# Kernel tuning notes

Hardware: AMD Instinct MI355X
Metric: run time of the kernel (lower is better)

The kernel has to match this reference:

```python
import jax, jax.numpy as jnp
import numpy as np

DIM = 2048
N_HEADS = 16
HEAD_DIM = DIM // N_HEADS
EPS = 1e-6


def setup_inputs() -> dict:
    key = jax.random.key(0)
    k1, k2, k3, k4, k5 = jax.random.split(key, 5)
    B, S = 2, 2048
    x = jax.random.normal(k1, (B, S, DIM), dtype=jnp.float32)
    cos = jax.random.uniform(k2, (S, HEAD_DIM), dtype=jnp.float32)
    sin = jax.random.uniform(k3, (S, HEAD_DIM), dtype=jnp.float32)
    # torch nn.Linear convention: weight [out_features, in_features], y = x @ W.T
    W_qkv = jax.random.normal(k4, (3 * DIM, DIM), dtype=jnp.float32) * 0.02
    W_proj = jax.random.normal(k5, (DIM, DIM), dtype=jnp.float32) * 0.02
    return {"x": x, "cos": cos, "sin": sin, "W_qkv": W_qkv, "W_proj": W_proj}


def _apply_rope(x, cos, sin):
    # x: [B,H,S,D], cos/sin: [S,D]; rotate interleaved even/odd pairs
    x1, x2 = x[..., ::2], x[..., 1::2]
    c = cos[:, ::2][None, None]  # [1,1,S,D/2]
    s = sin[:, ::2][None, None]
    y1 = x1 * c - x2 * s
    y2 = x1 * s + x2 * c
    return jnp.stack([y1, y2], axis=-1).reshape(x.shape)


def _rms_norm(x):
    # per-head RMS normalization over last dim, no learned scale
    return x * jax.lax.rsqrt(jnp.mean(x * x, axis=-1, keepdims=True) + EPS)


def reference(x, cos, sin, W_qkv, W_proj):
    b, s, d = x.shape
    qkv = jnp.einsum('bsd,ed->bse', x, W_qkv)  # [B,S,3*dim]
    q, k, v = jnp.split(qkv, 3, axis=-1)
    # [B,S,dim] -> [B,H,S,Dh]
    def to_heads(t):
        return t.reshape(b, s, N_HEADS, HEAD_DIM).transpose(0, 2, 1, 3)
    q, k, v = to_heads(q), to_heads(k), to_heads(v)
    q = _apply_rope(_rms_norm(q), cos, sin)
    k = _apply_rope(_rms_norm(k), cos, sin)
    scale = 1.0 / jnp.sqrt(jnp.asarray(HEAD_DIM, dtype=x.dtype))
    scores = jnp.einsum('bhqd,bhkd->bhqk', q, k) * scale  # [B,H,S,S]
    attn = jax.nn.softmax(scores, axis=-1)
    out = jnp.einsum('bhqk,bhkd->bhqd', attn, v)  # [B,H,S,Dh]
    out = out.transpose(0, 2, 1, 3).reshape(b, s, d)
    return jnp.einsum('bsd,od->bso', out, W_proj)
```

## Files before the change

### kernel.cpp

```cpp
#include <hip/hip_runtime.h>
#include <math.h>

#define BATCH 2
#define SEQ   2048
#define DIM   2048
#define NH    16
#define HD    128
#define EPS   1e-6f

typedef _Float16 f16x8 __attribute__((ext_vector_type(8)));
typedef _Float16 f16x4 __attribute__((ext_vector_type(4)));
typedef _Float16 f16x2 __attribute__((ext_vector_type(2)));
typedef float    f32x4 __attribute__((ext_vector_type(4)));

#define MFMA_F16 __builtin_amdgcn_mfma_f32_16x16x32_f16

__global__ __launch_bounds__(256) void cvt_all(
    const float* __restrict__ x, const float* __restrict__ wqkv,
    const float* __restrict__ wproj, _Float16* __restrict__ x16,
    _Float16* __restrict__ wh, _Float16* __restrict__ wph) {
  int bid = blockIdx.x;
  const float* in;
  _Float16* out;
  int i;
  if (bid < 8192)       { in = x;     out = x16; i = bid; }
  else if (bid < 20480) { in = wqkv;  out = wh;  i = bid - 8192; }
  else                  { in = wproj; out = wph; i = bid - 20480; }
  int j = i * 256 + threadIdx.x;
  float4 v = ((const float4*)in)[j];
  f16x4 o;
  o[0] = (_Float16)v.x; o[1] = (_Float16)v.y;
  o[2] = (_Float16)v.z; o[3] = (_Float16)v.w;
  ((f16x4*)out)[j] = o;
}

template <typename OT>
__global__ __launch_bounds__(512, 2) void gemm_1p(
    const _Float16* __restrict__ Ag, const _Float16* __restrict__ Bg,
    OT* __restrict__ C, int M, int N, int K) {
  __shared__ __align__(16) _Float16 smem[2][384][64];

  const int t = threadIdx.x;
  const int w = t >> 6, lane = t & 63;
  const int bm = blockIdx.y * 128, bn = blockIdx.x * 256;
  const int wr = (w >> 2) * 64;
  const int wc = (w & 3) * 64;
  const int quad = lane >> 4, c15 = lane & 15;

  const _Float16* baseA = Ag + (size_t)bm * K;
  const _Float16* baseB = Bg + (size_t)bn * K;

  const int lrow = lane >> 3;
  const int lswz = ((lane & 7) ^ lrow) * 8;

  const int col0 = ((0 + quad) ^ (c15 & 7)) * 8;
  const int col1 = ((4 + quad) ^ (c15 & 7)) * 8;

  f32x4 acc[4][4] = {};
  f16x8 a0[4], b0[4], a1[4], b1[4];

#define STAGE_TILE(buf, kofs)                                                  \
  {                                                                            \
    _Pragma("unroll")                                                          \
    for (int e = 0; e < 6; ++e) {                                              \
      int c = w * 6 + e;                                                       \
      int rl = c * 8 + lrow;                                                   \
      const _Float16* g = (rl < 128) ? (baseA + (size_t)rl * K)                \
                                     : (baseB + (size_t)(rl - 128) * K);       \
      __builtin_amdgcn_global_load_lds(                                        \
          (const __attribute__((address_space(1))) unsigned int*)(g + (kofs) + lswz), \
          (__attribute__((address_space(3))) unsigned int*)(&smem[buf][c * 8][0]),    \
          16, 0, 0);                                                           \
    }                                                                          \
  }

#define RD(dstA, dstB, colv, buf)                                              \
  _Pragma("unroll")                                                            \
  for (int m2 = 0; m2 < 4; ++m2)                                               \
    dstA[m2] = *(const f16x8*)(&smem[buf][wr + m2 * 16 + c15][colv]);          \
  _Pragma("unroll")                                                            \
  for (int n2 = 0; n2 < 4; ++n2)                                               \
    dstB[n2] = *(const f16x8*)(&smem[buf][128 + wc + n2 * 16 + c15][colv]);

#define MM(af, bf)                                                             \
  _Pragma("unroll")                                                            \
  for (int m2 = 0; m2 < 4; ++m2)                                               \
    _Pragma("unroll")                                                          \
    for (int n2 = 0; n2 < 4; ++n2)                                             \
      acc[m2][n2] = MFMA_F16(af[m2], bf[n2], acc[m2][n2], 0, 0, 0);

#define SB() __builtin_amdgcn_sched_barrier(0);

  STAGE_TILE(0, 0)
  asm volatile("s_waitcnt vmcnt(0)" ::: "memory");
  SB();
  __builtin_amdgcn_s_barrier();
  SB();
  STAGE_TILE(1, 64)
  RD(a0, b0, col0, 0);

  const int NT = K >> 6;
  for (int tt = 0; tt < NT; ++tt) {
    const int buf = tt & 1;
    RD(a1, b1, col1, buf);
    __builtin_amdgcn_s_setprio(1);
    MM(a0, b0);
    __builtin_amdgcn_s_setprio(0);
    asm volatile("s_waitcnt lgkmcnt(0)" ::: "memory");
    asm volatile("s_waitcnt vmcnt(0)" ::: "memory");
    SB();
    __builtin_amdgcn_s_barrier();
    SB();
    if (tt + 2 < NT) { STAGE_TILE(buf, (tt + 2) * 64) }
    if (tt + 1 < NT) { RD(a0, b0, col0, 1 - buf); }
    __builtin_amdgcn_s_setprio(1);
    MM(a1, b1);
    __builtin_amdgcn_s_setprio(0);
  }

  #pragma unroll
  for (int m2 = 0; m2 < 4; ++m2)
    #pragma unroll
    for (int n2 = 0; n2 < 4; ++n2) {
      int col = bn + wc + 16 * n2 + c15;
      #pragma unroll
      for (int r = 0; r < 4; ++r) {
        int row = bm + wr + 16 * m2 + quad * 4 + r;
        C[(size_t)row * N + col] = (OT)acc[m2][n2][r];
      }
    }
#undef STAGE_TILE
#undef RD
#undef MM
#undef SB
}

__global__ __launch_bounds__(256) void rope_vtrans(
    const _Float16* __restrict__ qkv, const float* __restrict__ cosb,
    const float* __restrict__ sinb, _Float16* __restrict__ Qg,
    _Float16* __restrict__ Kg, _Float16* __restrict__ Vt) {
  __shared__ _Float16 L[64 * 132];
  const int bid = blockIdx.x;
  const int t = threadIdx.x;
  if (bid < 4096) {
    const int b = bid >> 11, s = bid & (SEQ - 1);
    const int wave = t >> 6, lane = t & 63;
    const _Float16* base = qkv + (size_t)bid * (3 * DIM);
    const float c  = cosb[s * HD + 2 * lane];
    const float sn = sinb[s * HD + 2 * lane];
    #pragma unroll
    for (int h = wave; h < NH; h += 4) {
      f16x2 qv = *(const f16x2*)(base + h * HD + 2 * lane);
      f16x2 kv = *(const f16x2*)(base + DIM + h * HD + 2 * lane);
      float qx = (float)qv[0], qy = (float)qv[1];
      float kx = (float)kv[0], ky = (float)kv[1];
      float ssq = qx * qx + qy * qy;
      float ssk = kx * kx + ky * ky;
      #pragma unroll
      for (int off = 32; off >= 1; off >>= 1) {
        ssq += __shfl_xor(ssq, off, 64);
        ssk += __shfl_xor(ssk, off, 64);
      }
      float rq = rsqrtf(ssq * (1.0f / HD) + EPS);
      float rk = rsqrtf(ssk * (1.0f / HD) + EPS);
      float q1 = qx * rq, q2 = qy * rq;
      float k1 = kx * rk, k2 = ky * rk;
      float qy1 = q1 * c - q2 * sn, qy2 = q1 * sn + q2 * c;
      float ky1 = k1 * c - k2 * sn, ky2 = k1 * sn + k2 * c;
      size_t o = ((size_t)(b * NH + h) * SEQ + s) * HD + 2 * lane;
      f16x2 qo, ko;
      qo[0] = (_Float16)qy1; qo[1] = (_Float16)qy2;
      ko[0] = (_Float16)ky1; ko[1] = (_Float16)ky2;
      *(f16x2*)(Qg + o) = qo;
      *(f16x2*)(Kg + o) = ko;
    }
  } else {
    const int vb = bid - 4096;
    const int s0 = (vb & 31) * 64, h = (vb >> 5) & 15, b = vb >> 9;
    const _Float16* src =
        qkv + ((size_t)(b * SEQ + s0)) * (3 * DIM) + 2 * DIM + h * HD;
    #pragma unroll
    for (int it = 0; it < 4; ++it) {
      int f = t + it * 256;
      int r = f >> 4, c8 = f & 15;
      f16x8 v = *(const f16x8*)(src + (size_t)r * (3 * DIM) + c8 * 8);
      *(f16x8*)(&L[r * 132 + c8 * 8]) = v;
    }
    __syncthreads();
    const int d = t >> 1, sc = (t & 1) * 32;
    size_t dst = ((size_t)((b * NH + h) * HD + d)) * SEQ + s0 + sc;
    #pragma unroll
    for (int j = 0; j < 8; ++j) {
      f16x4 o;
      o[0] = L[(sc + 4 * j + 0) * 132 + d];
      o[1] = L[(sc + 4 * j + 1) * 132 + d];
      o[2] = L[(sc + 4 * j + 2) * 132 + d];
      o[3] = L[(sc + 4 * j + 3) * 132 + d];
      *(f16x4*)(Vt + dst + j * 4) = o;
    }
  }
}

#define QT 128
#define KC 32

__global__ __launch_bounds__(256, 2) void flash_f16(
    const _Float16* __restrict__ Qg, const _Float16* __restrict__ Kg,
    const _Float16* __restrict__ Vtg, _Float16* __restrict__ Og) {
  __shared__ __align__(16) _Float16 sm[21504];

  const int t = threadIdx.x, w = t >> 6, lane = t & 63;
  const int quad = lane >> 4, c15 = lane & 15;
  const int bid = blockIdx.x;
  const int grp = (bid & 7) * 4 + ((bid >> 3) >> 4);
  const int qi  = (bid >> 3) & 15;
  const int bh = grp;
  const int hy = grp & (NH - 1), bz = grp >> 4;
  const int q0 = qi * QT;
  const int wr = w * 32;

  {
    const _Float16* qsrc = Qg + ((size_t)bh * SEQ + q0) * HD;
    #pragma unroll
    for (int p = 0; p < 8; ++p) {
      int ci = p * 256 + t;
      int r = ci >> 4, c8 = (ci & 15) ^ (r & 15);
      __builtin_amdgcn_global_load_lds(
          (const __attribute__((address_space(1))) unsigned int*)(qsrc + (size_t)r * HD + c8 * 8),
          (__attribute__((address_space(3))) unsigned int*)(sm + ci * 8), 16, 0, 0);
    }
  }
  __syncthreads();
  f16x8 qf[2][4];
  #pragma unroll
  for (int mf = 0; mf < 2; ++mf)
    #pragma unroll
    for (int ks = 0; ks < 4; ++ks) {
      int m = wr + mf * 16 + c15;
      int c8 = ks * 4 + quad;
      qf[mf][ks] = *(const f16x8*)(sm + (m * 16 + (c8 ^ (m & 15))) * 8);
    }
  asm volatile("s_waitcnt lgkmcnt(0)" ::: "memory");
  __builtin_amdgcn_sched_barrier(0);
  __syncthreads();

  float lrow[8];
  f32x4 oacc[2][8];
  #pragma unroll
  for (int i = 0; i < 8; ++i) lrow[i] = 0.f;
  #pragma unroll
  for (int mf = 0; mf < 2; ++mf)
    #pragma unroll
    for (int nf = 0; nf < 8; ++nf) oacc[mf][nf] = (f32x4){0.f, 0.f, 0.f, 0.f};

  const float sl = 0.12751744f;
  const float M2 = 16.322231f;
  _Float16* Pw = sm + 16384 + w * 1280;

#define STAGE_KV(buf, kk)                                                     \
  _Pragma("unroll")                                                           \
  for (int e = 0; e < 4; ++e) {                                               \
    int idx = w * 4 + e;                                                      \
    int tile = idx >> 3, p = idx & 7;                                         \
    int ci = p * 64 + lane;                                                   \
    if (tile == 0) {                                                          \
      int r = ci >> 4, c8 = (ci & 15) ^ (r & 15);                             \
      int rp = 2 * (r & 15) + (r >> 4);                                       \
      const _Float16* src = Kg +                                              \
          ((size_t)bh * SEQ + (kk) + rp) * HD + c8 * 8;                       \
      __builtin_amdgcn_global_load_lds(                                       \
          (const __attribute__((address_space(1))) unsigned int*)src,         \
          (__attribute__((address_space(3))) unsigned int*)                   \
              (sm + (buf) * 4096 + ci * 8), 16, 0, 0);                        \
    } else {                                                                  \
      int d = ci >> 2, c8 = (ci & 3) ^ (d & 3);                               \
      const _Float16* src = Vtg + (size_t)bh * HD * SEQ + (size_t)d * SEQ     \
          + (kk) + c8 * 8;                                                    \
      __builtin_amdgcn_global_load_lds(                                       \
          (const __attribute__((address_space(1))) unsigned int*)src,         \
          (__attribute__((address_space(3))) unsigned int*)                   \
              (sm + 8192 + (buf) * 4096 + ci * 8), 16, 0, 0);                 \
    }                                                                         \
  }

  STAGE_KV(0, 0)

  const int NC = SEQ / KC;
  for (int it = 0; it < NC; ++it) {
    const int cur = it & 1, cb0 = cur * 4096;
    asm volatile("s_waitcnt vmcnt(0)" ::: "memory");
    __builtin_amdgcn_sched_barrier(0);
    __builtin_amdgcn_s_barrier();
    __builtin_amdgcn_sched_barrier(0);
    if (it + 1 < NC) { STAGE_KV(1 - cur, (it + 1) * KC) }

    f32x4 accs[2][2] = {};
    #pragma unroll
    for (int nf = 0; nf < 2; ++nf) {
      f16x8 kh[4];
      #pragma unroll
      for (int ks = 0; ks < 4; ++ks) {
        int n = nf * 16 + c15;
        int c8 = ks * 4 + quad;
        kh[ks] = *(const f16x8*)(sm + cb0 + (n * 16 + (c8 ^ (n & 15))) * 8);
      }
      __builtin_amdgcn_s_setprio(1);
      #pragma unroll
      for (int ks = 0; ks < 4; ++ks) {
        accs[0][nf] = MFMA_F16(qf[0][ks], kh[ks], accs[0][nf], 0, 0, 0);
        accs[1][nf] = MFMA_F16(qf[1][ks], kh[ks], accs[1][nf], 0, 0, 0);
      }
      __builtin_amdgcn_s_setprio(0);
    }

    #pragma unroll
    for (int mf = 0; mf < 2; ++mf)
      #pragma unroll
      for (int reg = 0; reg < 4; ++reg) {
        float p0 = exp2f(fmaf(accs[mf][0][reg], sl, -M2));
        float p1 = exp2f(fmaf(accs[mf][1][reg], sl, -M2));
        lrow[mf * 4 + reg] += p0 + p1;
        int prow = mf * 16 + quad * 4 + reg;
        f16x2 pp;
        pp[0] = (_Float16)p0; pp[1] = (_Float16)p1;
        *(f16x2*)(Pw + prow * 40 + 2 * c15) = pp;
      }

    f16x8 pa0 = *(const f16x8*)(Pw + (c15) * 40 + quad * 8);
    f16x8 pa1 = *(const f16x8*)(Pw + (16 + c15) * 40 + quad * 8);
    __builtin_amdgcn_s_setprio(1);
    #pragma unroll
    for (int nf = 0; nf < 8; ++nf) {
      int dd = nf * 16 + c15;
      int slot = (dd * 4 + (quad ^ (dd & 3))) * 8;
      f16x8 vv = *(const f16x8*)(sm + 8192 + cb0 + slot);
      oacc[0][nf] = MFMA_F16(pa0, vv, oacc[0][nf], 0, 0, 0);
      oacc[1][nf] = MFMA_F16(pa1, vv, oacc[1][nf], 0, 0, 0);
    }
    __builtin_amdgcn_s_setprio(0);
  }

  #pragma unroll
  for (int i = 0; i < 8; ++i) {
    float s = lrow[i];
    #pragma unroll
    for (int off = 8; off >= 1; off >>= 1) s += __shfl_xor(s, off, 64);
    lrow[i] = s;
  }
  #pragma unroll
  for (int mf = 0; mf < 2; ++mf)
    #pragma unroll
    for (int reg = 0; reg < 4; ++reg) {
      float inv = 1.0f / lrow[mf * 4 + reg];
      int row = q0 + wr + mf * 16 + quad * 4 + reg;
      size_t ob = ((size_t)bz * SEQ + row) * DIM + hy * HD + c15;
      #pragma unroll
      for (int nf = 0; nf < 8; ++nf)
        Og[ob + nf * 16] = (_Float16)(oacc[mf][nf][reg] * inv);
    }
#undef STAGE_KV
}

extern "C" void kernel_launch(void* const* d_in, const int* in_sizes, int n_in,
                              void* d_out, int out_size, void* d_ws, size_t ws_size,
                              hipStream_t stream) {
  const float* x     = (const float*)d_in[0];
  const float* cosb  = (const float*)d_in[1];
  const float* sinb  = (const float*)d_in[2];
  const float* Wqkv  = (const float*)d_in[3];
  const float* Wproj = (const float*)d_in[4];
  float* out = (float*)d_out;

  char* ws = (char*)d_ws;
  _Float16* qkv16 = (_Float16*)ws;
  char* R = ws + 100663296;
  _Float16* x16 = (_Float16*)(R);
  _Float16* Wh  = (_Float16*)(R + 16777216);
  _Float16* Wph = (_Float16*)(R + 41943040);
  _Float16* Q16 = (_Float16*)(R);
  _Float16* K16 = (_Float16*)(R + 16777216);
  _Float16* Vt  = (_Float16*)(R + 50331648);
  _Float16* O16 = (_Float16*)(ws);

  cvt_all<<<24576, 256, 0, stream>>>(x, Wqkv, Wproj, x16, Wh, Wph);
  gemm_1p<_Float16><<<dim3(24, 32), 512, 0, stream>>>(x16, Wh, qkv16, 4096, 6144, 2048);
  rope_vtrans<<<5120, 256, 0, stream>>>(qkv16, cosb, sinb, Q16, K16, Vt);
  flash_f16<<<512, 256, 0, stream>>>(Q16, K16, Vt, O16);
  gemm_1p<float><<<dim3(8, 32), 512, 0, stream>>>(O16, Wph, out, 4096, 2048, 2048);
}
```

Measured before the change: 398.9 us.

## Fuse RMSNorm, RoPE and V transpose into the QKV GEMM epilogue

The QKV projection GEMM now writes Q and K directly, applying per-head RMS normalization (reducing across waves through shared memory) and interleaved RoPE in its epilogue. It also writes V transposed via an LDS staging buffer. This removes the separate rope_vtrans kernel and the round trip of the full fp16 qkv tensor through global memory. In exchange the GEMM epilogue gains extra barriers, shuffles, uncoalesced cos/sin loads and strided 4-byte stores, plus a different workspace layout.

Result: slower. 413.6 us (+3.7%).

```diff
diff --git a/kernel.cpp b/kernel.cpp
--- a/kernel.cpp
+++ b/kernel.cpp
@@ -34,29 +34,20 @@
   ((f16x4*)out)[j] = o;
 }
 
-template <typename OT>
-__global__ __launch_bounds__(512, 2) void gemm_1p(
-    const _Float16* __restrict__ Ag, const _Float16* __restrict__ Bg,
-    OT* __restrict__ C, int M, int N, int K) {
-  __shared__ __align__(16) _Float16 smem[2][384][64];
-
-  const int t = threadIdx.x;
-  const int w = t >> 6, lane = t & 63;
-  const int bm = blockIdx.y * 128, bn = blockIdx.x * 256;
-  const int wr = (w >> 2) * 64;
-  const int wc = (w & 3) * 64;
-  const int quad = lane >> 4, c15 = lane & 15;
-
-  const _Float16* baseA = Ag + (size_t)bm * K;
-  const _Float16* baseB = Bg + (size_t)bn * K;
-
-  const int lrow = lane >> 3;
-  const int lswz = ((lane & 7) ^ lrow) * 8;
-
-  const int col0 = ((0 + quad) ^ (c15 & 7)) * 8;
-  const int col1 = ((4 + quad) ^ (c15 & 7)) * 8;
-
-  f32x4 acc[4][4] = {};
+#define GEMM_PREAMBLE()                                                        \
+  const int t = threadIdx.x;                                                   \
+  const int w = t >> 6, lane = t & 63;                                         \
+  const int bm = blockIdx.y * 128, bn = blockIdx.x * 256;                      \
+  const int wr = (w >> 2) * 64;                                                \
+  const int wc = (w & 3) * 64;                                                 \
+  const int quad = lane >> 4, c15 = lane & 15;                                 \
+  const _Float16* baseA = Ag + (size_t)bm * K;                                 \
+  const _Float16* baseB = Bg + (size_t)bn * K;                                 \
+  const int lrow = lane >> 3;                                                  \
+  const int lswz = ((lane & 7) ^ lrow) * 8;                                    \
+  const int col0 = ((0 + quad) ^ (c15 & 7)) * 8;                               \
+  const int col1 = ((4 + quad) ^ (c15 & 7)) * 8;                               \
+  f32x4 acc[4][4] = {};                                                        \
   f16x8 a0[4], b0[4], a1[4], b1[4];
 
 #define STAGE_TILE(buf, kofs)                                                  \
@@ -91,33 +82,135 @@
 
 #define SB() __builtin_amdgcn_sched_barrier(0);
 
-  STAGE_TILE(0, 0)
-  asm volatile("s_waitcnt vmcnt(0)" ::: "memory");
-  SB();
-  __builtin_amdgcn_s_barrier();
-  SB();
-  STAGE_TILE(1, 64)
-  RD(a0, b0, col0, 0);
-
-  const int NT = K >> 6;
-  for (int tt = 0; tt < NT; ++tt) {
-    const int buf = tt & 1;
-    RD(a1, b1, col1, buf);
-    __builtin_amdgcn_s_setprio(1);
-    MM(a0, b0);
-    __builtin_amdgcn_s_setprio(0);
-    asm volatile("s_waitcnt lgkmcnt(0)" ::: "memory");
-    asm volatile("s_waitcnt vmcnt(0)" ::: "memory");
-    SB();
-    __builtin_amdgcn_s_barrier();
-    SB();
-    if (tt + 2 < NT) { STAGE_TILE(buf, (tt + 2) * 64) }
-    if (tt + 1 < NT) { RD(a0, b0, col0, 1 - buf); }
-    __builtin_amdgcn_s_setprio(1);
-    MM(a1, b1);
-    __builtin_amdgcn_s_setprio(0);
-  }
-
+#define GEMM_MAINLOOP()                                                        \
+  STAGE_TILE(0, 0)                                                             \
+  asm volatile("s_waitcnt vmcnt(0)" ::: "memory");                             \
+  SB();                                                                        \
+  __builtin_amdgcn_s_barrier();                                                \
+  SB();                                                                        \
+  STAGE_TILE(1, 64)                                                            \
+  RD(a0, b0, col0, 0);                                                         \
+  const int NT = K >> 6;                                                       \
+  for (int tt = 0; tt < NT; ++tt) {                                            \
+    const int buf = tt & 1;                                                    \
+    RD(a1, b1, col1, buf);                                                     \
+    __builtin_amdgcn_s_setprio(1);                                             \
+    MM(a0, b0);                                                                \
+    __builtin_amdgcn_s_setprio(0);                                             \
+    asm volatile("s_waitcnt lgkmcnt(0)" ::: "memory");                         \
+    asm volatile("s_waitcnt vmcnt(0)" ::: "memory");                           \
+    SB();                                                                      \
+    __builtin_amdgcn_s_barrier();                                              \
+    SB();                                                                      \
+    if (tt + 2 < NT) { STAGE_TILE(buf, (tt + 2) * 64) }                        \
+    if (tt + 1 < NT) { RD(a0, b0, col0, 1 - buf); }                            \
+    __builtin_amdgcn_s_setprio(1);                                             \
+    MM(a1, b1);                                                                \
+    __builtin_amdgcn_s_setprio(0);                                             \
+  }
+
+__global__ __launch_bounds__(512, 2) void gemm_qkv(
+    const _Float16* __restrict__ Ag, const _Float16* __restrict__ Bg,
+    const float* __restrict__ cosb, const float* __restrict__ sinb,
+    _Float16* __restrict__ Qg, _Float16* __restrict__ Kg,
+    _Float16* __restrict__ Vt, int K) {
+  __shared__ __align__(16) _Float16 smem[2][384][64];
+  GEMM_PREAMBLE()
+  GEMM_MAINLOOP()
+
+  const int region = bn >> 11;
+  const int b = bm >> 11;
+  const int s0 = bm & (SEQ - 1);
+
+  if (region < 2) {
+    float* LDSf = (float*)smem;
+    float ps[4][4];
+    #pragma unroll
+    for (int m2 = 0; m2 < 4; ++m2)
+      #pragma unroll
+      for (int r = 0; r < 4; ++r) {
+        float p = 0.f;
+        #pragma unroll
+        for (int n = 0; n < 4; ++n) p += acc[m2][n][r] * acc[m2][n][r];
+        #pragma unroll
+        for (int off = 8; off >= 1; off >>= 1) p += __shfl_xor(p, off, 64);
+        ps[m2][r] = p;
+      }
+    __syncthreads();
+    if (c15 == 0) {
+      #pragma unroll
+      for (int m2 = 0; m2 < 4; ++m2)
+        #pragma unroll
+        for (int r = 0; r < 4; ++r)
+          LDSf[w * 64 + 16 * m2 + quad * 4 + r] = ps[m2][r];
+    }
+    __syncthreads();
+    _Float16* dst = (region == 0) ? Qg : Kg;
+    const int h = ((bn & (2 * DIM - 1)) >> 7) & 15;
+    const int hh = h + (wc >> 7);
+    const int dbase = wc & 64;
+    #pragma unroll
+    for (int m2 = 0; m2 < 4; ++m2)
+      #pragma unroll
+      for (int r = 0; r < 4; ++r) {
+        float tot = ps[m2][r] + LDSf[(w ^ 1) * 64 + 16 * m2 + quad * 4 + r];
+        float rsq = rsqrtf(tot * (1.0f / HD) + EPS);
+        int s = s0 + wr + 16 * m2 + quad * 4 + r;
+        #pragma unroll
+        for (int n = 0; n < 4; ++n) {
+          int dh = dbase + 16 * n + c15;
+          float v = acc[m2][n][r] * rsq;
+          float vp = __shfl_xor(v, 1, 64);
+          float cs = cosb[s * HD + (dh & ~1)];
+          float sn = sinb[s * HD + (dh & ~1)];
+          float y = ((c15 & 1) == 0) ? (v * cs - vp * sn) : (vp * sn + v * cs);
+          float yp = __shfl_xor(y, 1, 64);
+          if ((c15 & 1) == 0) {
+            f16x2 o2;
+            o2[0] = (_Float16)y; o2[1] = (_Float16)yp;
+            *(f16x2*)(dst + ((size_t)(b * NH + hh) * SEQ + s) * HD + dh) = o2;
+          }
+        }
+      }
+  } else {
+    _Float16* Lh = (_Float16*)smem;
+    const int hv0 = ((bn & (2 * DIM - 1)) >> 7) & 15;
+    const int d_out = t & 127;
+    const int sq0 = (t >> 7) * 32;
+    #pragma unroll
+    for (int half = 0; half < 2; ++half) {
+      __syncthreads();
+      if ((wc >> 7) == half) {
+        #pragma unroll
+        for (int m2 = 0; m2 < 4; ++m2)
+          #pragma unroll
+          for (int n = 0; n < 4; ++n)
+            #pragma unroll
+            for (int r = 0; r < 4; ++r)
+              Lh[(wr + 16 * m2 + quad * 4 + r) * 132 + (wc & 64) + 16 * n + c15] =
+                  (_Float16)acc[m2][n][r];
+      }
+      __syncthreads();
+      size_t dst = ((size_t)(b * NH + hv0 + half) * HD + d_out) * SEQ + s0 + sq0;
+      #pragma unroll
+      for (int j = 0; j < 8; ++j) {
+        f16x4 o;
+        o[0] = Lh[(sq0 + 4 * j + 0) * 132 + d_out];
+        o[1] = Lh[(sq0 + 4 * j + 1) * 132 + d_out];
+        o[2] = Lh[(sq0 + 4 * j + 2) * 132 + d_out];
+        o[3] = Lh[(sq0 + 4 * j + 3) * 132 + d_out];
+        *(f16x4*)(Vt + dst + 4 * j) = o;
+      }
+    }
+  }
+}
+
+__global__ __launch_bounds__(512, 2) void gemm_proj(
+    const _Float16* __restrict__ Ag, const _Float16* __restrict__ Bg,
+    float* __restrict__ C, int N, int K) {
+  __shared__ __align__(16) _Float16 smem[2][384][64];
+  GEMM_PREAMBLE()
+  GEMM_MAINLOOP()
   #pragma unroll
   for (int m2 = 0; m2 < 4; ++m2)
     #pragma unroll
@@ -126,79 +219,9 @@
       #pragma unroll
       for (int r = 0; r < 4; ++r) {
         int row = bm + wr + 16 * m2 + quad * 4 + r;
-        C[(size_t)row * N + col] = (OT)acc[m2][n2][r];
-      }
-    }
-#undef STAGE_TILE
-#undef RD
-#undef MM
-#undef SB
-}
-
-__global__ __launch_bounds__(256) void rope_vtrans(
-    const _Float16* __restrict__ qkv, const float* __restrict__ cosb,
-    const float* __restrict__ sinb, _Float16* __restrict__ Qg,
-    _Float16* __restrict__ Kg, _Float16* __restrict__ Vt) {
-  __shared__ _Float16 L[64 * 132];
-  const int bid = blockIdx.x;
-  const int t = threadIdx.x;
-  if (bid < 4096) {
-    const int b = bid >> 11, s = bid & (SEQ - 1);
-    const int wave = t >> 6, lane = t & 63;
-    const _Float16* base = qkv + (size_t)bid * (3 * DIM);
-    const float c  = cosb[s * HD + 2 * lane];
-    const float sn = sinb[s * HD + 2 * lane];
-    #pragma unroll
-    for (int h = wave; h < NH; h += 4) {
-      f16x2 qv = *(const f16x2*)(base + h * HD + 2 * lane);
-      f16x2 kv = *(const f16x2*)(base + DIM + h * HD + 2 * lane);
-      float qx = (float)qv[0], qy = (float)qv[1];
-      float kx = (float)kv[0], ky = (float)kv[1];
-      float ssq = qx * qx + qy * qy;
-      float ssk = kx * kx + ky * ky;
-      #pragma unroll
-      for (int off = 32; off >= 1; off >>= 1) {
-        ssq += __shfl_xor(ssq, off, 64);
-        ssk += __shfl_xor(ssk, off, 64);
-      }
-      float rq = rsqrtf(ssq * (1.0f / HD) + EPS);
-      float rk = rsqrtf(ssk * (1.0f / HD) + EPS);
-      float q1 = qx * rq, q2 = qy * rq;
-      float k1 = kx * rk, k2 = ky * rk;
-      float qy1 = q1 * c - q2 * sn, qy2 = q1 * sn + q2 * c;
-      float ky1 = k1 * c - k2 * sn, ky2 = k1 * sn + k2 * c;
-      size_t o = ((size_t)(b * NH + h) * SEQ + s) * HD + 2 * lane;
-      f16x2 qo, ko;
-      qo[0] = (_Float16)qy1; qo[1] = (_Float16)qy2;
-      ko[0] = (_Float16)ky1; ko[1] = (_Float16)ky2;
-      *(f16x2*)(Qg + o) = qo;
-      *(f16x2*)(Kg + o) = ko;
-    }
-  } else {
-    const int vb = bid - 4096;
-    const int s0 = (vb & 31) * 64, h = (vb >> 5) & 15, b = vb >> 9;
-    const _Float16* src =
-        qkv + ((size_t)(b * SEQ + s0)) * (3 * DIM) + 2 * DIM + h * HD;
-    #pragma unroll
-    for (int it = 0; it < 4; ++it) {
-      int f = t + it * 256;
-      int r = f >> 4, c8 = f & 15;
-      f16x8 v = *(const f16x8*)(src + (size_t)r * (3 * DIM) + c8 * 8);
-      *(f16x8*)(&L[r * 132 + c8 * 8]) = v;
-    }
-    __syncthreads();
-    const int d = t >> 1, sc = (t & 1) * 32;
-    size_t dst = ((size_t)((b * NH + h) * HD + d)) * SEQ + s0 + sc;
-    #pragma unroll
-    for (int j = 0; j < 8; ++j) {
-      f16x4 o;
-      o[0] = L[(sc + 4 * j + 0) * 132 + d];
-      o[1] = L[(sc + 4 * j + 1) * 132 + d];
-      o[2] = L[(sc + 4 * j + 2) * 132 + d];
-      o[3] = L[(sc + 4 * j + 3) * 132 + d];
-      *(f16x4*)(Vt + dst + j * 4) = o;
-    }
-  }
+        C[(size_t)row * N + col] = acc[m2][n2][r];
+      }
+    }
 }
 
 #define QT 128
@@ -372,19 +395,17 @@
   float* out = (float*)d_out;
 
   char* ws = (char*)d_ws;
-  _Float16* qkv16 = (_Float16*)ws;
+  _Float16* Q16 = (_Float16*)(ws);
+  _Float16* O16 = (_Float16*)(ws + 16777216);
+  _Float16* K16 = (_Float16*)(ws + 33554432);
+  _Float16* Vt  = (_Float16*)(ws + 50331648);
   char* R = ws + 100663296;
   _Float16* x16 = (_Float16*)(R);
   _Float16* Wh  = (_Float16*)(R + 16777216);
   _Float16* Wph = (_Float16*)(R + 41943040);
-  _Float16* Q16 = (_Float16*)(R);
-  _Float16* K16 = (_Float16*)(R + 16777216);
-  _Float16* Vt  = (_Float16*)(R + 50331648);
-  _Float16* O16 = (_Float16*)(ws);
 
   cvt_all<<<24576, 256, 0, stream>>>(x, Wqkv, Wproj, x16, Wh, Wph);
-  gemm_1p<_Float16><<<dim3(24, 32), 512, 0, stream>>>(x16, Wh, qkv16, 4096, 6144, 2048);
-  rope_vtrans<<<5120, 256, 0, stream>>>(qkv16, cosb, sinb, Q16, K16, Vt);
+  gemm_qkv<<<dim3(24, 32), 512, 0, stream>>>(x16, Wh, cosb, sinb, Q16, K16, Vt, 2048);
   flash_f16<<<512, 256, 0, stream>>>(Q16, K16, Vt, O16);
-  gemm_1p<float><<<dim3(8, 32), 512, 0, stream>>>(O16, Wph, out, 4096, 2048, 2048);
+  gemm_proj<<<dim3(8, 32), 512, 0, stream>>>(O16, Wph, out, 2048, 2048);
 }
```
